# Kernel tuning notes

Measured on AMD Instinct MI355X. Metric: run time of the kernel, lower is better.

The kernel has to match this reference:

```python
import jax, jax.numpy as jnp
import numpy as np

T = 32.0                       # softmax temperature
THRESH = float(np.cos(np.pi * 40.0 / 180.0))  # cos(degree), degree=40
NEG_INF = -9.0e15


def setup_inputs() -> dict:
    key = jax.random.key(0)
    ks = jax.random.split(key, 11)
    B, C, D_IMG, D_ATT, H_ATT, H = 2048, 1000, 2048, 312, 128, 128
    def rn(k, shape, scale=1.0):
        return jax.random.normal(k, shape, dtype=jnp.float32) * scale
    return {
        "image_feats": rn(ks[0], (B, D_IMG)),
        "img_proto":   rn(ks[1], (C, D_IMG)),
        "attributes":  rn(ks[2], (C, D_ATT)),
        "unused":      0,
        # parameters
        "att_g":   rn(ks[3], (D_ATT, H_ATT), 0.05),
        "slim_w":  rn(ks[4], (D_IMG, D_ATT), 0.02),   # proto_slim weight (transposed torch layout)
        "slim_b":  rn(ks[5], (D_ATT,), 0.02),
        "img_w":   rn(ks[6], (D_IMG, H), 0.02),
        "proto_w": rn(ks[7], (2 * D_ATT, H), 0.02),   # att_dim + proto_red_dim = 624
        "proto_b": rn(ks[8], (1, H), 0.02),
        "fc_w":    rn(ks[9], (H, 1), 0.05),
        "fc_b":    rn(ks[10], (1,), 0.05),
    }


def reference(image_feats, img_proto, attributes, unused,
              att_g, slim_w, slim_b, img_w, proto_w, proto_b, fc_w, fc_b):
    # proto_slim: [C, D_img] -> [C, att_dim]
    proto_red = img_proto @ slim_w + slim_b

    # --- get_attention: cosine similarity among attribute projections ---
    g = attributes @ att_g                                   # [C, att_hC] (g == h in original)
    gn = g / jnp.clip(jnp.linalg.norm(g, axis=1, keepdims=True), 1e-12)
    sim = gn @ gn.T                                          # [C, C] cosine similarity
    raw = jnp.where(sim > THRESH, sim, NEG_INF)              # threshold mask
    attn = jax.nn.softmax(raw * T, axis=1)                   # [C, C]

    # --- propagate prototypes ---
    att_outs = attn @ attributes                             # [C, att_dim]
    img_proto_outs = attn @ proto_red                        # [C, att_dim]
    outs = jnp.concatenate([att_outs, img_proto_outs], axis=1)  # [C, 2*att_dim]

    # --- relation MLP (broadcast instead of materialized expand+matmul) ---
    img_h = image_feats @ img_w                              # [B, H]
    proto_h = outs @ proto_w                                 # [C, H]
    hidden = jax.nn.relu(img_h[:, None, :] + proto_h[None, :, :] + proto_b)  # [B, C, H]
    outputs = hidden @ fc_w + fc_b                           # [B, C, 1]
    return outputs[..., 0]                                   # [B, C]
```

## Files before the change

### kernel.cpp

```cpp
#include <hip/hip_runtime.h>

typedef unsigned short ushort_t;
typedef __bf16 bf16x8 __attribute__((ext_vector_type(8)));
typedef float f32x4 __attribute__((ext_vector_type(4)));
typedef float f32x2 __attribute__((ext_vector_type(2)));
typedef ushort_t us4 __attribute__((ext_vector_type(4)));

#define T_SOFT 32.0f
#define THRESH 0.76604444311897803f
#define SW 1048

__device__ __forceinline__ ushort_t f2bf(float f) {
  union { float f; unsigned u; } x; x.f = f;
  unsigned r = (x.u + 0x7fffu + ((x.u >> 16) & 1u)) >> 16;
  return (ushort_t)r;
}
__device__ __forceinline__ float bf2f(ushort_t h) {
  union { unsigned u; float f; } x; x.u = ((unsigned)h) << 16; return x.f;
}

__device__ __forceinline__ us4 pack4(float4 x) {
  union { unsigned u[2]; us4 h; } r;
  union { float4 f; unsigned u[4]; } a;
  a.f = x;
  r.u[0] = __builtin_amdgcn_perm(a.u[1] + 0x8000u, a.u[0] + 0x8000u, 0x07060302u);
  r.u[1] = __builtin_amdgcn_perm(a.u[3] + 0x8000u, a.u[2] + 0x8000u, 0x07060302u);
  return r.h;
}

__global__ __launch_bounds__(256) void tr3_k(const float* __restrict__ s0, ushort_t* __restrict__ d0,
                                             const float* __restrict__ s1, ushort_t* __restrict__ d1,
                                             const float* __restrict__ s2, ushort_t* __restrict__ d2,
                                             const float* __restrict__ s3, ushort_t* __restrict__ d3,
                                             float* __restrict__ z0, float* __restrict__ z1,
                                             ushort_t* __restrict__ gn_bf) {
  int b = blockIdx.x, tid = threadIdx.x;
  if (b >= 1296) {
    if (b < 1360) {
      int local = b - 1296;
      float4 z = make_float4(0.f, 0.f, 0.f, 0.f);
      float4* p = reinterpret_cast<float4*>(z0) + local * 1024 + tid;
      p[0] = z; p[256] = z; p[512] = z; p[768] = z;
    } else if (b < 1437) {
      int local = b - 1360;
      float4 z = make_float4(0.f, 0.f, 0.f, 0.f);
      float4* p = reinterpret_cast<float4*>(z1);
      int base = local * 1024 + tid;
      #pragma unroll
      for (int i = 0; i < 4; ++i) { int idx = base + i * 256; if (idx < 78000) p[idx] = z; }
    } else {
      us4 z = {0, 0, 0, 0};
      *reinterpret_cast<us4*>(gn_bf + 1000 * 128 + tid * 4) = z;
    }
    return;
  }
  __shared__ float tl[32][33];
  const float* src; ushort_t* dst; int R, C, Rpad, local, ctiles;
  if (b < 640)       { src = s0; dst = d0; R = 2048; C = 312; Rpad = 2048; local = b;        ctiles = 10; }
  else if (b < 896)  { src = s1; dst = d1; R = 2048; C = 128; Rpad = 2048; local = b - 640;  ctiles = 4;  }
  else if (b < 976)  { src = s2; dst = d2; R = 624;  C = 128; Rpad = 640;  local = b - 896;  ctiles = 4;  }
  else               { src = s3; dst = d3; R = 1000; C = 312; Rpad = 1024; local = b - 976;  ctiles = 10; }
  int rt = local / ctiles, ct = local - rt * ctiles;
  int r0 = rt * 32, c0 = ct * 32;
  #pragma unroll
  for (int p = 0; p < 4; ++p) {
    int idx = p * 256 + tid;
    int rr = idx >> 5, cc = idx & 31;
    float v = 0.f;
    if (r0 + rr < R && c0 + cc < C) v = src[(size_t)(r0 + rr) * C + (c0 + cc)];
    tl[cc][rr] = v;
  }
  __syncthreads();
  int cc = tid >> 3, rq = tid & 7;
  if (c0 + cc < C) {
    us4 o;
    o[0] = f2bf(tl[cc][rq * 4 + 0]);
    o[1] = f2bf(tl[cc][rq * 4 + 1]);
    o[2] = f2bf(tl[cc][rq * 4 + 2]);
    o[3] = f2bf(tl[cc][rq * 4 + 3]);
    *reinterpret_cast<us4*>(dst + (size_t)(c0 + cc) * Rpad + r0 + rq * 4) = o;
  }
}

template <int NCT>
__device__ __forceinline__ void gemm_seg(
    const float* __restrict__ A, int M, int lda,
    const ushort_t* __restrict__ BT, int ldbt,
    float* __restrict__ C, int N,
    int r0, int c0, int k0, int nsteps,
    ushort_t* __restrict__ As, ushort_t* __restrict__ Bs, int tid) {
  const int SA = 72;
  const int BP = NCT / 2;
  int lane = tid & 63, wv = tid >> 6;
  int l15 = lane & 15, quad = lane >> 4;
  int arow = tid >> 4, akq = tid & 15;
  int brow = tid >> 3, bkq = tid & 7;

  const float* agp[8];
  #pragma unroll
  for (int p = 0; p < 8; ++p) {
    int r = r0 + arow + p * 16; if (r >= M) r = M - 1;
    agp[p] = A + (size_t)r * lda + k0 + akq * 4;
  }
  const ushort_t* bgp[BP];
  #pragma unroll
  for (int p = 0; p < BP; ++p)
    bgp[p] = BT + (size_t)(c0 + brow + p * 32) * ldbt + k0 + bkq * 8;

  float4 ap[8]; bf16x8 bp[BP];
  #pragma unroll
  for (int p = 0; p < 8; ++p) ap[p] = *reinterpret_cast<const float4*>(agp[p]);
  #pragma unroll
  for (int p = 0; p < BP; ++p) bp[p] = *reinterpret_cast<const bf16x8*>(bgp[p]);

  f32x4 acc[2][NCT];
  #pragma unroll
  for (int i = 0; i < 2; ++i)
    #pragma unroll
    for (int j = 0; j < NCT; ++j) acc[i][j] = f32x4{0.f, 0.f, 0.f, 0.f};

  for (int s = 0; s < nsteps; ++s) {
    if (s) __syncthreads();
    #pragma unroll
    for (int p = 0; p < 8; ++p)
      *reinterpret_cast<us4*>(As + (arow + p * 16) * SA + akq * 4) = pack4(ap[p]);
    #pragma unroll
    for (int p = 0; p < BP; ++p)
      *reinterpret_cast<bf16x8*>(Bs + (brow + p * 32) * SA + bkq * 8) = bp[p];
    if (s + 1 < nsteps) {
      #pragma unroll
      for (int p = 0; p < 8; ++p) ap[p] = *reinterpret_cast<const float4*>(agp[p] + 64);
      #pragma unroll
      for (int p = 0; p < BP; ++p) bp[p] = *reinterpret_cast<const bf16x8*>(bgp[p] + 64);
      #pragma unroll
      for (int p = 0; p < 8; ++p) agp[p] += 64;
      #pragma unroll
      for (int p = 0; p < BP; ++p) bgp[p] += 64;
    }
    __syncthreads();
    #pragma unroll
    for (int kh = 0; kh < 2; ++kh) {
      bf16x8 af[2];
      #pragma unroll
      for (int pi = 0; pi < 2; ++pi)
        af[pi] = *reinterpret_cast<bf16x8*>(As + ((wv * 2 + pi) * 16 + l15) * SA + kh * 32 + quad * 8);
      #pragma unroll
      for (int ct = 0; ct < NCT; ++ct) {
        bf16x8 bfr = *reinterpret_cast<bf16x8*>(Bs + (ct * 16 + l15) * SA + kh * 32 + quad * 8);
        acc[0][ct] = __builtin_amdgcn_mfma_f32_16x16x32_bf16(af[0], bfr, acc[0][ct], 0, 0, 0);
        acc[1][ct] = __builtin_amdgcn_mfma_f32_16x16x32_bf16(af[1], bfr, acc[1][ct], 0, 0, 0);
      }
    }
  }
  #pragma unroll
  for (int pi = 0; pi < 2; ++pi) {
    #pragma unroll
    for (int ct = 0; ct < NCT; ++ct) {
      int col = c0 + ct * 16 + l15;
      if (col < N) {
        #pragma unroll
        for (int r = 0; r < 4; ++r) {
          int row = r0 + (wv * 2 + pi) * 16 + quad * 4 + r;
          if (row < M) atomicAdd(&C[(size_t)row * N + col], acc[pi][ct][r]);
        }
      }
    }
  }
}

__global__ __launch_bounds__(256) void mega_k(
    const float* __restrict__ attributes, const float* __restrict__ att_g,
    ushort_t* __restrict__ gn_bf,
    const float* __restrict__ img_proto, const ushort_t* __restrict__ slimT,
    float* __restrict__ proto_red,
    const float* __restrict__ image_feats, const ushort_t* __restrict__ imgwT,
    float* __restrict__ img_h) {
  __shared__ ushort_t As[128 * 72];
  __shared__ ushort_t Bs[128 * 72];
  int b = blockIdx.x, tid = threadIdx.x;
  if (b < 125) {
    __shared__ float a_lds[8][316];
    __shared__ float red2[8][2];
    int h = tid & 127;
    int c0 = b * 8;
    for (int idx = tid; idx < 8 * 312; idx += 256) {
      int r = idx / 312;
      int k = idx - r * 312;
      a_lds[r][k] = attributes[(c0 + r) * 312 + k];
    }
    __syncthreads();
    float acc[8] = {0.f,0.f,0.f,0.f,0.f,0.f,0.f,0.f};
    for (int k = 0; k < 312; k += 4) {
      float w0 = att_g[(k + 0) * 128 + h];
      float w1 = att_g[(k + 1) * 128 + h];
      float w2 = att_g[(k + 2) * 128 + h];
      float w3 = att_g[(k + 3) * 128 + h];
      #pragma unroll
      for (int r = 0; r < 8; ++r) {
        float4 a4 = *reinterpret_cast<const float4*>(&a_lds[r][k]);
        acc[r] += a4.x * w0 + a4.y * w1 + a4.z * w2 + a4.w * w3;
      }
    }
    int lane = tid & 63, wvid = (tid >> 6) & 1;
    #pragma unroll
    for (int r = 0; r < 8; ++r) {
      float v = acc[r] * acc[r];
      #pragma unroll
      for (int off = 32; off > 0; off >>= 1) v += __shfl_xor(v, off, 64);
      if (lane == 0) red2[r][wvid] = v;
    }
    __syncthreads();
    #pragma unroll
    for (int r = 0; r < 8; ++r) {
      float nrm = fmaxf(sqrtf(red2[r][0] + red2[r][1]), 1e-12f);
      gn_bf[(c0 + r) * 128 + h] = f2bf(acc[r] / nrm);
    }
    return;
  }
  b -= 125;
  if (b < 64) {
    int rb = b >> 2, kc = b & 3;
    gemm_seg<8>(image_feats, 2048, 2048, imgwT, 2048, img_h, 128,
                rb * 128, 0, kc * 512, 8, As, Bs, tid);
  } else {
    b -= 64;
    int kc = b & 3; int t = b >> 2;
    int rb = t / 3, cb = t - rb * 3;
    if (cb == 2)
      gemm_seg<4>(img_proto, 1000, 2048, slimT, 2048, proto_red, 312,
                  rb * 128, 256, kc * 512, 8, As, Bs, tid);
    else
      gemm_seg<8>(img_proto, 1000, 2048, slimT, 2048, proto_red, 312,
                  rb * 128, cb * 128, kc * 512, 8, As, Bs, tid);
  }
}

__global__ __launch_bounds__(256) void trp_k(const float* __restrict__ proto_red,
                                             ushort_t* __restrict__ poutT) {
  int b = blockIdx.x, tid = threadIdx.x;
  if (b >= 320) {
    int local = b - 320;
    us4 z = {0, 0, 0, 0};
    ushort_t* base = poutT + 624ull * 1024 + local * 4096;
    *reinterpret_cast<us4*>(base + tid * 16)      = z;
    *reinterpret_cast<us4*>(base + tid * 16 + 4)  = z;
    *reinterpret_cast<us4*>(base + tid * 16 + 8)  = z;
    *reinterpret_cast<us4*>(base + tid * 16 + 12) = z;
    return;
  }
  __shared__ float tl[32][33];
  int rt = b / 10, ct = b - rt * 10;
  int r0 = rt * 32, c0 = ct * 32;
  #pragma unroll
  for (int p = 0; p < 4; ++p) {
    int idx = p * 256 + tid;
    int rr = idx >> 5, cc = idx & 31;
    float v = 0.f;
    if (r0 + rr < 1000 && c0 + cc < 312) v = proto_red[(size_t)(r0 + rr) * 312 + (c0 + cc)];
    tl[cc][rr] = v;
  }
  __syncthreads();
  int cc = tid >> 3, rq = tid & 7;
  if (c0 + cc < 312) {
    us4 o;
    o[0] = f2bf(tl[cc][rq * 4 + 0]);
    o[1] = f2bf(tl[cc][rq * 4 + 1]);
    o[2] = f2bf(tl[cc][rq * 4 + 2]);
    o[3] = f2bf(tl[cc][rq * 4 + 3]);
    *reinterpret_cast<us4*>(poutT + (size_t)(312 + c0 + cc) * 1024 + r0 + rq * 4) = o;
  }
}

__global__ __launch_bounds__(256) void attn3_k(
    const ushort_t* __restrict__ gn_bf, const ushort_t* __restrict__ poutT,
    const float* __restrict__ slim_b, ushort_t* __restrict__ outs) {
  __shared__ ushort_t W[16 * SW];
  __shared__ float rsum[16];
  __shared__ int flags[63];
  int tid = threadIdx.x;
  int i0 = blockIdx.x * 16;
  int lane = tid & 63, wv = tid >> 6;
  int l15 = lane & 15, quad = lane >> 4;
  if (tid < 63) flags[tid] = 0;
  if (tid >= 64 && tid < 80) rsum[tid - 64] = 0.f;
  W[(tid >> 4) * SW + 1008 + (tid & 15)] = 0;
  __syncthreads();

  const ushort_t* abase = gn_bf + (size_t)(i0 + l15) * 128 + quad * 8;
  bf16x8 af0 = *reinterpret_cast<const bf16x8*>(abase);
  bf16x8 af1 = *reinterpret_cast<const bf16x8*>(abase + 32);
  bf16x8 af2 = *reinterpret_cast<const bf16x8*>(abase + 64);
  bf16x8 af3 = *reinterpret_cast<const bf16x8*>(abase + 96);
  float rs[4] = {0.f, 0.f, 0.f, 0.f};
  for (int jt = wv; jt < 63; jt += 4) {
    const ushort_t* bbase = gn_bf + (size_t)(jt * 16 + l15) * 128 + quad * 8;
    f32x4 d = {0.f, 0.f, 0.f, 0.f};
    d = __builtin_amdgcn_mfma_f32_16x16x32_bf16(af0, *reinterpret_cast<const bf16x8*>(bbase),      d, 0, 0, 0);
    d = __builtin_amdgcn_mfma_f32_16x16x32_bf16(af1, *reinterpret_cast<const bf16x8*>(bbase + 32), d, 0, 0, 0);
    d = __builtin_amdgcn_mfma_f32_16x16x32_bf16(af2, *reinterpret_cast<const bf16x8*>(bbase + 64), d, 0, 0, 0);
    d = __builtin_amdgcn_mfma_f32_16x16x32_bf16(af3, *reinterpret_cast<const bf16x8*>(bbase + 96), d, 0, 0, 0);
    int hot = 0;
    #pragma unroll
    for (int r = 0; r < 4; ++r) {
      float w = 0.f;
      if (d[r] > THRESH) { w = __expf(T_SOFT * (d[r] - 1.0f)); hot = 1; }
      ushort_t wb = f2bf(w);
      W[(quad * 4 + r) * SW + jt * 16 + l15] = wb;
      rs[r] += bf2f(wb);
    }
    if (hot) flags[jt] = 1;
  }
  #pragma unroll
  for (int r = 0; r < 4; ++r) {
    float v = rs[r];
    v += __shfl_xor(v, 1, 64); v += __shfl_xor(v, 2, 64);
    v += __shfl_xor(v, 4, 64); v += __shfl_xor(v, 8, 64);
    if (l15 == 0) atomicAdd(&rsum[quad * 4 + r], v);
  }
  __syncthreads();

  f32x4 acc[10];
  #pragma unroll
  for (int t = 0; t < 10; ++t) acc[t] = f32x4{0.f, 0.f, 0.f, 0.f};
  for (int s = 0; s < 32; ++s) {
    int f = flags[2 * s] | ((2 * s + 1 < 63) ? flags[2 * s + 1] : 0);
    if (!f) continue;
    bf16x8 a = *reinterpret_cast<bf16x8*>(W + l15 * SW + s * 32 + quad * 8);
    #pragma unroll
    for (int t = 0; t < 10; ++t) {
      int nrow = (wv * 10 + t) * 16 + l15;
      bf16x8 bfr = *reinterpret_cast<const bf16x8*>(poutT + (size_t)nrow * 1024 + s * 32 + quad * 8);
      acc[t] = __builtin_amdgcn_mfma_f32_16x16x32_bf16(a, bfr, acc[t], 0, 0, 0);
    }
  }
  #pragma unroll
  for (int t = 0; t < 10; ++t) {
    int col = (wv * 10 + t) * 16 + l15;
    float bias = (col >= 312 && col < 624) ? slim_b[col - 312] : 0.f;
    #pragma unroll
    for (int r = 0; r < 4; ++r) {
      int gi = i0 + quad * 4 + r;
      if (gi < 1000) {
        float inv = 1.f / fmaxf(rsum[quad * 4 + r], 1e-30f);
        outs[(size_t)gi * 640 + col] = f2bf(acc[t][r] * inv + bias);
      }
    }
  }
}

__global__ __launch_bounds__(256) void mfma_gemm_bt(
    const ushort_t* __restrict__ A, const ushort_t* __restrict__ BT,
    float* __restrict__ C, int M, int N, int K, int Mt, int Nt,
    const float* __restrict__ bias) {
  int wid = blockIdx.x * 4 + (threadIdx.x >> 6);
  int lane = threadIdx.x & 63;
  int tm = wid / Nt;
  int tn = wid - tm * Nt;
  if (tm >= Mt) return;
  int l15 = lane & 15;
  int quad = lane >> 4;
  const bf16x8* ap = reinterpret_cast<const bf16x8*>(A + (size_t)(tm * 16 + l15) * K + quad * 8);
  const bf16x8* bp = reinterpret_cast<const bf16x8*>(BT + (size_t)(tn * 16 + l15) * K + quad * 8);
  f32x4 acc = {0.f, 0.f, 0.f, 0.f};
  for (int s = 0, steps = K >> 7; s < steps; ++s) {
    bf16x8 a0 = ap[0],  b0 = bp[0];
    bf16x8 a1 = ap[4],  b1 = bp[4];
    bf16x8 a2 = ap[8],  b2 = bp[8];
    bf16x8 a3 = ap[12], b3 = bp[12];
    ap += 16; bp += 16;
    acc = __builtin_amdgcn_mfma_f32_16x16x32_bf16(a0, b0, acc, 0, 0, 0);
    acc = __builtin_amdgcn_mfma_f32_16x16x32_bf16(a1, b1, acc, 0, 0, 0);
    acc = __builtin_amdgcn_mfma_f32_16x16x32_bf16(a2, b2, acc, 0, 0, 0);
    acc = __builtin_amdgcn_mfma_f32_16x16x32_bf16(a3, b3, acc, 0, 0, 0);
  }
  int col = tn * 16 + l15;
  if (col >= N) return;
  float bv = bias ? bias[col] : 0.f;
  int row0 = tm * 16 + quad * 4;
  #pragma unroll
  for (int r = 0; r < 4; ++r) {
    int row = row0 + r;
    if (row < M) C[(size_t)row * N + col] = acc[r] + bv;
  }
}

__global__ __launch_bounds__(256) void final_k(
    const float* __restrict__ img_h, const float* __restrict__ ph,
    const float* __restrict__ fc_w, const float* __restrict__ fc_b,
    float* __restrict__ out) {
  __shared__ float ih[128][132];
  __shared__ float ps[64][132];
  __shared__ float ws_[128];
  int tid = threadIdx.x;
  int b0 = blockIdx.x * 128;
  int c0 = blockIdx.y * 64;
  for (int idx = tid; idx < 4096; idx += 256) {
    int row = idx >> 5, c4 = (idx & 31) * 4;
    float4 v = *reinterpret_cast<const float4*>(img_h + (size_t)(b0 + row) * 128 + c4);
    *reinterpret_cast<float4*>(&ih[row][c4]) = v;
  }
  for (int idx = tid; idx < 2048; idx += 256) {
    int row = idx >> 5, c4 = (idx & 31) * 4;
    int c = c0 + row;
    float4 v = make_float4(0.f, 0.f, 0.f, 0.f);
    if (c < 1000) v = *reinterpret_cast<const float4*>(ph + (size_t)c * 128 + c4);
    *reinterpret_cast<float4*>(&ps[row][c4]) = v;
  }
  if (tid < 128) ws_[tid] = fc_w[tid];
  __syncthreads();
  int tx = tid & 15, ty = tid >> 4;
  f32x2 acc[8][4] = {};
  const f32x2 zero2 = {0.f, 0.f};
  for (int h = 0; h < 128; h += 4) {
    float4 w4 = *reinterpret_cast<float4*>(&ws_[h]);
    f32x2 wlo = {w4.x, w4.y}, whi = {w4.z, w4.w};
    float4 a4[8], p4[4];
    #pragma unroll
    for (int i = 0; i < 8; ++i) a4[i] = *reinterpret_cast<float4*>(&ih[ty * 8 + i][h]);
    #pragma unroll
    for (int j = 0; j < 4; ++j) p4[j] = *reinterpret_cast<float4*>(&ps[tx * 4 + j][h]);
    #pragma unroll
    for (int i = 0; i < 8; ++i) {
      f32x2 alo = {a4[i].x, a4[i].y}, ahi = {a4[i].z, a4[i].w};
      #pragma unroll
      for (int j = 0; j < 4; ++j) {
        f32x2 plo = {p4[j].x, p4[j].y}, phi = {p4[j].z, p4[j].w};
        f32x2 t0 = __builtin_elementwise_max(alo + plo, zero2);
        f32x2 t1 = __builtin_elementwise_max(ahi + phi, zero2);
        acc[i][j] = acc[i][j] + t0 * wlo;
        acc[i][j] = acc[i][j] + t1 * whi;
      }
    }
  }
  float fb = fc_b[0];
  #pragma unroll
  for (int i = 0; i < 8; ++i) {
    int b = b0 + ty * 8 + i;
    int c = c0 + tx * 4;
    if (c < 1000) {
      float4 v = make_float4(acc[i][0].x + acc[i][0].y + fb, acc[i][1].x + acc[i][1].y + fb,
                             acc[i][2].x + acc[i][2].y + fb, acc[i][3].x + acc[i][3].y + fb);
      *reinterpret_cast<float4*>(out + (size_t)b * 1000 + c) = v;
    }
  }
}

extern "C" void kernel_launch(void* const* d_in, const int* in_sizes, int n_in,
                              void* d_out, int out_size, void* d_ws, size_t ws_size,
                              hipStream_t stream) {
  const float* image_feats = (const float*)d_in[0];
  const float* img_proto   = (const float*)d_in[1];
  const float* attributes  = (const float*)d_in[2];
  const float* att_g   = (const float*)d_in[4];
  const float* slim_w  = (const float*)d_in[5];
  const float* slim_b  = (const float*)d_in[6];
  const float* img_w   = (const float*)d_in[7];
  const float* proto_w = (const float*)d_in[8];
  const float* proto_b = (const float*)d_in[9];
  const float* fc_w    = (const float*)d_in[10];
  const float* fc_b    = (const float*)d_in[11];
  float* out = (float*)d_out;

  char* ws = (char*)d_ws;
  size_t o = 0;
  auto alloc = [&](size_t bytes) { size_t r = o; o += (bytes + 255) & ~(size_t)255; return r; };
  ushort_t* imgwT   = (ushort_t*)(ws + alloc(128ull * 2048 * 2));
  ushort_t* slimT   = (ushort_t*)(ws + alloc(320ull * 2048 * 2));
  ushort_t* protowT = (ushort_t*)(ws + alloc(128ull * 640 * 2));
  ushort_t* gn_bf   = (ushort_t*)(ws + alloc(1008ull * 128 * 2));
  float* proto_red = (float*)(ws + alloc(1000ull * 312 * 4));
  ushort_t* poutT   = (ushort_t*)(ws + alloc(640ull * 1024 * 2));
  ushort_t* outs_bf = (ushort_t*)(ws + alloc(1008ull * 640 * 2));
  float* img_h     = (float*)(ws + alloc(2048ull * 128 * 4));
  float* ph        = (float*)(ws + alloc(1000ull * 128 * 4));

  tr3_k<<<1438, 256, 0, stream>>>(slim_w, slimT, img_w, imgwT, proto_w, protowT,
                                  attributes, poutT, img_h, proto_red, gn_bf);

  mega_k<<<285, 256, 0, stream>>>(attributes, att_g, gn_bf,
                                  img_proto, slimT, proto_red,
                                  image_feats, imgwT, img_h);

  trp_k<<<324, 256, 0, stream>>>(proto_red, poutT);

  attn3_k<<<63, 256, 0, stream>>>(gn_bf, poutT, slim_b, outs_bf);

  mfma_gemm_bt<<<126, 256, 0, stream>>>(outs_bf, protowT, ph, 1000, 128, 640, 63, 8, proto_b);

  final_k<<<dim3(16, 16), 256, 0, stream>>>(img_h, ph, fc_w, fc_b, out);
}
```

Before: 182.7 us.

## Fuse proto transpose into GEMM, drop split-K atomics, fuse proto_w GEMM into attention

The proto_red GEMM is now computed in transposed form (slimT times img_proto^T) and written straight to poutT as bf16, which removes the separate transpose kernel and the fp32 proto_red buffer. The img_h and proto GEMMs no longer split K four ways with atomicAdd, so the zeroing blocks go away, but each block now runs the full K=2048 loop with fewer blocks in flight. The outs @ proto_w GEMM is fused into the attention kernel through a shared-memory staging tile, which removes the outs_bf round trip and one launch. Together this cuts the pipeline from six launches to four, at the cost of less parallelism in the big GEMMs.

```diff
diff --git a/kernel.cpp b/kernel.cpp
--- a/kernel.cpp
+++ b/kernel.cpp
@@ -9,6 +9,7 @@
 #define T_SOFT 32.0f
 #define THRESH 0.76604444311897803f
 #define SW 1048
+#define SO 648
 
 __device__ __forceinline__ ushort_t f2bf(float f) {
   union { float f; unsigned u; } x; x.f = f;
@@ -32,34 +33,25 @@
                                              const float* __restrict__ s1, ushort_t* __restrict__ d1,
                                              const float* __restrict__ s2, ushort_t* __restrict__ d2,
                                              const float* __restrict__ s3, ushort_t* __restrict__ d3,
-                                             float* __restrict__ z0, float* __restrict__ z1,
-                                             ushort_t* __restrict__ gn_bf) {
+                                             ushort_t* __restrict__ gn_bf, ushort_t* __restrict__ poutT) {
   int b = blockIdx.x, tid = threadIdx.x;
   if (b >= 1296) {
-    if (b < 1360) {
-      int local = b - 1296;
-      float4 z = make_float4(0.f, 0.f, 0.f, 0.f);
-      float4* p = reinterpret_cast<float4*>(z0) + local * 1024 + tid;
-      p[0] = z; p[256] = z; p[512] = z; p[768] = z;
-    } else if (b < 1437) {
-      int local = b - 1360;
-      float4 z = make_float4(0.f, 0.f, 0.f, 0.f);
-      float4* p = reinterpret_cast<float4*>(z1);
-      int base = local * 1024 + tid;
-      #pragma unroll
-      for (int i = 0; i < 4; ++i) { int idx = base + i * 256; if (idx < 78000) p[idx] = z; }
+    us4 z = {0, 0, 0, 0};
+    if (b == 1296) {
+      *reinterpret_cast<us4*>(gn_bf + 1000 * 128 + tid * 4) = z;
     } else {
-      us4 z = {0, 0, 0, 0};
-      *reinterpret_cast<us4*>(gn_bf + 1000 * 128 + tid * 4) = z;
+      ushort_t* base = poutT + 632ull * 1024 + tid * 32;
+      #pragma unroll
+      for (int i = 0; i < 8; ++i) *reinterpret_cast<us4*>(base + i * 4) = z;
     }
     return;
   }
   __shared__ float tl[32][33];
-  const float* src; ushort_t* dst; int R, C, Rpad, local, ctiles;
-  if (b < 640)       { src = s0; dst = d0; R = 2048; C = 312; Rpad = 2048; local = b;        ctiles = 10; }
-  else if (b < 896)  { src = s1; dst = d1; R = 2048; C = 128; Rpad = 2048; local = b - 640;  ctiles = 4;  }
-  else if (b < 976)  { src = s2; dst = d2; R = 624;  C = 128; Rpad = 640;  local = b - 896;  ctiles = 4;  }
-  else               { src = s3; dst = d3; R = 1000; C = 312; Rpad = 1024; local = b - 976;  ctiles = 10; }
+  const float* src; ushort_t* dst; int R, C, Cw, Rpad, local, ctiles;
+  if (b < 640)       { src = s0; dst = d0; R = 2048; C = 312; Cw = 320; Rpad = 2048; local = b;       ctiles = 10; }
+  else if (b < 896)  { src = s1; dst = d1; R = 2048; C = 128; Cw = 128; Rpad = 2048; local = b - 640; ctiles = 4;  }
+  else if (b < 976)  { src = s2; dst = d2; R = 624;  C = 128; Cw = 128; Rpad = 640;  local = b - 896; ctiles = 4;  }
+  else               { src = s3; dst = d3; R = 1000; C = 312; Cw = 312; Rpad = 1024; local = b - 976; ctiles = 10; }
   int rt = local / ctiles, ct = local - rt * ctiles;
   int r0 = rt * 32, c0 = ct * 32;
   #pragma unroll
@@ -72,7 +64,7 @@
   }
   __syncthreads();
   int cc = tid >> 3, rq = tid & 7;
-  if (c0 + cc < C) {
+  if (c0 + cc < Cw) {
     us4 o;
     o[0] = f2bf(tl[cc][rq * 4 + 0]);
     o[1] = f2bf(tl[cc][rq * 4 + 1]);
@@ -82,60 +74,50 @@
   }
 }
 
-template <int NCT>
-__device__ __forceinline__ void gemm_seg(
-    const float* __restrict__ A, int M, int lda,
-    const ushort_t* __restrict__ BT, int ldbt,
-    float* __restrict__ C, int N,
-    int r0, int c0, int k0, int nsteps,
-    ushort_t* __restrict__ As, ushort_t* __restrict__ Bs, int tid) {
+__device__ __forceinline__ void gemm_imgh(const float* __restrict__ A, const ushort_t* __restrict__ BT,
+                                          float* __restrict__ C, int r0,
+                                          ushort_t* __restrict__ As, ushort_t* __restrict__ Bs, int tid) {
   const int SA = 72;
-  const int BP = NCT / 2;
   int lane = tid & 63, wv = tid >> 6;
   int l15 = lane & 15, quad = lane >> 4;
   int arow = tid >> 4, akq = tid & 15;
   int brow = tid >> 3, bkq = tid & 7;
-
   const float* agp[8];
   #pragma unroll
-  for (int p = 0; p < 8; ++p) {
-    int r = r0 + arow + p * 16; if (r >= M) r = M - 1;
-    agp[p] = A + (size_t)r * lda + k0 + akq * 4;
-  }
-  const ushort_t* bgp[BP];
-  #pragma unroll
-  for (int p = 0; p < BP; ++p)
-    bgp[p] = BT + (size_t)(c0 + brow + p * 32) * ldbt + k0 + bkq * 8;
-
-  float4 ap[8]; bf16x8 bp[BP];
+  for (int p = 0; p < 8; ++p) agp[p] = A + (size_t)(r0 + arow + p * 16) * 2048 + akq * 4;
+  const ushort_t* bgp[4];
+  #pragma unroll
+  for (int p = 0; p < 4; ++p) bgp[p] = BT + (size_t)(brow + p * 32) * 2048 + bkq * 8;
+
+  float4 ap[8]; bf16x8 bp[4];
   #pragma unroll
   for (int p = 0; p < 8; ++p) ap[p] = *reinterpret_cast<const float4*>(agp[p]);
   #pragma unroll
-  for (int p = 0; p < BP; ++p) bp[p] = *reinterpret_cast<const bf16x8*>(bgp[p]);
-
-  f32x4 acc[2][NCT];
+  for (int p = 0; p < 4; ++p) bp[p] = *reinterpret_cast<const bf16x8*>(bgp[p]);
+
+  f32x4 acc[2][8];
   #pragma unroll
   for (int i = 0; i < 2; ++i)
     #pragma unroll
-    for (int j = 0; j < NCT; ++j) acc[i][j] = f32x4{0.f, 0.f, 0.f, 0.f};
-
-  for (int s = 0; s < nsteps; ++s) {
+    for (int j = 0; j < 8; ++j) acc[i][j] = f32x4{0.f, 0.f, 0.f, 0.f};
+
+  for (int s = 0; s < 32; ++s) {
     if (s) __syncthreads();
     #pragma unroll
     for (int p = 0; p < 8; ++p)
       *reinterpret_cast<us4*>(As + (arow + p * 16) * SA + akq * 4) = pack4(ap[p]);
     #pragma unroll
-    for (int p = 0; p < BP; ++p)
+    for (int p = 0; p < 4; ++p)
       *reinterpret_cast<bf16x8*>(Bs + (brow + p * 32) * SA + bkq * 8) = bp[p];
-    if (s + 1 < nsteps) {
+    if (s + 1 < 32) {
       #pragma unroll
       for (int p = 0; p < 8; ++p) ap[p] = *reinterpret_cast<const float4*>(agp[p] + 64);
       #pragma unroll
-      for (int p = 0; p < BP; ++p) bp[p] = *reinterpret_cast<const bf16x8*>(bgp[p] + 64);
+      for (int p = 0; p < 4; ++p) bp[p] = *reinterpret_cast<const bf16x8*>(bgp[p] + 64);
       #pragma unroll
       for (int p = 0; p < 8; ++p) agp[p] += 64;
       #pragma unroll
-      for (int p = 0; p < BP; ++p) bgp[p] += 64;
+      for (int p = 0; p < 4; ++p) bgp[p] += 64;
     }
     __syncthreads();
     #pragma unroll
@@ -145,7 +127,7 @@
       for (int pi = 0; pi < 2; ++pi)
         af[pi] = *reinterpret_cast<bf16x8*>(As + ((wv * 2 + pi) * 16 + l15) * SA + kh * 32 + quad * 8);
       #pragma unroll
-      for (int ct = 0; ct < NCT; ++ct) {
+      for (int ct = 0; ct < 8; ++ct) {
         bf16x8 bfr = *reinterpret_cast<bf16x8*>(Bs + (ct * 16 + l15) * SA + kh * 32 + quad * 8);
         acc[0][ct] = __builtin_amdgcn_mfma_f32_16x16x32_bf16(af[0], bfr, acc[0][ct], 0, 0, 0);
         acc[1][ct] = __builtin_amdgcn_mfma_f32_16x16x32_bf16(af[1], bfr, acc[1][ct], 0, 0, 0);
@@ -153,28 +135,104 @@
     }
   }
   #pragma unroll
-  for (int pi = 0; pi < 2; ++pi) {
-    #pragma unroll
-    for (int ct = 0; ct < NCT; ++ct) {
-      int col = c0 + ct * 16 + l15;
-      if (col < N) {
+  for (int pi = 0; pi < 2; ++pi)
+    #pragma unroll
+    for (int ct = 0; ct < 8; ++ct) {
+      int col = ct * 16 + l15;
+      #pragma unroll
+      for (int r = 0; r < 4; ++r) {
+        int row = r0 + (wv * 2 + pi) * 16 + quad * 4 + r;
+        C[(size_t)row * 128 + col] = acc[pi][ct][r];
+      }
+    }
+}
+
+__device__ __forceinline__ void gemm_protoT(const ushort_t* __restrict__ A, const float* __restrict__ B,
+                                            ushort_t* __restrict__ poutT, int r0, int c0,
+                                            ushort_t* __restrict__ As, ushort_t* __restrict__ Bs, int tid) {
+  const int SA = 72;
+  int lane = tid & 63, wv = tid >> 6;
+  int l15 = lane & 15, quad = lane >> 4;
+  int frow = tid >> 4, fkq = tid & 15;
+  int hrow = tid >> 3, hkq = tid & 7;
+  const ushort_t* agp[4];
+  #pragma unroll
+  for (int p = 0; p < 4; ++p) {
+    int r = r0 + hrow + p * 32; if (r >= 320) r = 319;
+    agp[p] = A + (size_t)r * 2048 + hkq * 8;
+  }
+  const float* bgp[8];
+  #pragma unroll
+  for (int p = 0; p < 8; ++p) {
+    int n = c0 + frow + p * 16; if (n >= 1000) n = 999;
+    bgp[p] = B + (size_t)n * 2048 + fkq * 4;
+  }
+  bf16x8 ar[4]; float4 br[8];
+  #pragma unroll
+  for (int p = 0; p < 4; ++p) ar[p] = *reinterpret_cast<const bf16x8*>(agp[p]);
+  #pragma unroll
+  for (int p = 0; p < 8; ++p) br[p] = *reinterpret_cast<const float4*>(bgp[p]);
+
+  f32x4 acc[2][8];
+  #pragma unroll
+  for (int i = 0; i < 2; ++i)
+    #pragma unroll
+    for (int j = 0; j < 8; ++j) acc[i][j] = f32x4{0.f, 0.f, 0.f, 0.f};
+
+  for (int s = 0; s < 32; ++s) {
+    if (s) __syncthreads();
+    #pragma unroll
+    for (int p = 0; p < 4; ++p)
+      *reinterpret_cast<bf16x8*>(As + (hrow + p * 32) * SA + hkq * 8) = ar[p];
+    #pragma unroll
+    for (int p = 0; p < 8; ++p)
+      *reinterpret_cast<us4*>(Bs + (frow + p * 16) * SA + fkq * 4) = pack4(br[p]);
+    if (s + 1 < 32) {
+      #pragma unroll
+      for (int p = 0; p < 4; ++p) ar[p] = *reinterpret_cast<const bf16x8*>(agp[p] + 64);
+      #pragma unroll
+      for (int p = 0; p < 8; ++p) br[p] = *reinterpret_cast<const float4*>(bgp[p] + 64);
+      #pragma unroll
+      for (int p = 0; p < 4; ++p) agp[p] += 64;
+      #pragma unroll
+      for (int p = 0; p < 8; ++p) bgp[p] += 64;
+    }
+    __syncthreads();
+    #pragma unroll
+    for (int kh = 0; kh < 2; ++kh) {
+      bf16x8 af[2];
+      #pragma unroll
+      for (int pi = 0; pi < 2; ++pi)
+        af[pi] = *reinterpret_cast<bf16x8*>(As + ((wv * 2 + pi) * 16 + l15) * SA + kh * 32 + quad * 8);
+      #pragma unroll
+      for (int ct = 0; ct < 8; ++ct) {
+        bf16x8 bfr = *reinterpret_cast<bf16x8*>(Bs + (ct * 16 + l15) * SA + kh * 32 + quad * 8);
+        acc[0][ct] = __builtin_amdgcn_mfma_f32_16x16x32_bf16(af[0], bfr, acc[0][ct], 0, 0, 0);
+        acc[1][ct] = __builtin_amdgcn_mfma_f32_16x16x32_bf16(af[1], bfr, acc[1][ct], 0, 0, 0);
+      }
+    }
+  }
+  #pragma unroll
+  for (int pi = 0; pi < 2; ++pi)
+    #pragma unroll
+    for (int ct = 0; ct < 8; ++ct) {
+      int n = c0 + ct * 16 + l15;
+      if (n < 1000) {
         #pragma unroll
         for (int r = 0; r < 4; ++r) {
-          int row = r0 + (wv * 2 + pi) * 16 + quad * 4 + r;
-          if (row < M) atomicAdd(&C[(size_t)row * N + col], acc[pi][ct][r]);
+          int m = r0 + (wv * 2 + pi) * 16 + quad * 4 + r;
+          if (m < 320) poutT[(size_t)(312 + m) * 1024 + n] = f2bf(acc[pi][ct][r]);
         }
       }
     }
-  }
 }
 
 __global__ __launch_bounds__(256) void mega_k(
     const float* __restrict__ attributes, const float* __restrict__ att_g,
     ushort_t* __restrict__ gn_bf,
     const float* __restrict__ img_proto, const ushort_t* __restrict__ slimT,
-    float* __restrict__ proto_red,
     const float* __restrict__ image_feats, const ushort_t* __restrict__ imgwT,
-    float* __restrict__ img_h) {
+    float* __restrict__ img_h, ushort_t* __restrict__ poutT) {
   __shared__ ushort_t As[128 * 72];
   __shared__ ushort_t Bs[128 * 72];
   int b = blockIdx.x, tid = threadIdx.x;
@@ -218,63 +276,21 @@
     return;
   }
   b -= 125;
-  if (b < 64) {
-    int rb = b >> 2, kc = b & 3;
-    gemm_seg<8>(image_feats, 2048, 2048, imgwT, 2048, img_h, 128,
-                rb * 128, 0, kc * 512, 8, As, Bs, tid);
+  if (b < 16) {
+    gemm_imgh(image_feats, imgwT, img_h, b * 128, As, Bs, tid);
   } else {
-    b -= 64;
-    int kc = b & 3; int t = b >> 2;
-    int rb = t / 3, cb = t - rb * 3;
-    if (cb == 2)
-      gemm_seg<4>(img_proto, 1000, 2048, slimT, 2048, proto_red, 312,
-                  rb * 128, 256, kc * 512, 8, As, Bs, tid);
-    else
-      gemm_seg<8>(img_proto, 1000, 2048, slimT, 2048, proto_red, 312,
-                  rb * 128, cb * 128, kc * 512, 8, As, Bs, tid);
-  }
-}
-
-__global__ __launch_bounds__(256) void trp_k(const float* __restrict__ proto_red,
-                                             ushort_t* __restrict__ poutT) {
-  int b = blockIdx.x, tid = threadIdx.x;
-  if (b >= 320) {
-    int local = b - 320;
-    us4 z = {0, 0, 0, 0};
-    ushort_t* base = poutT + 624ull * 1024 + local * 4096;
-    *reinterpret_cast<us4*>(base + tid * 16)      = z;
-    *reinterpret_cast<us4*>(base + tid * 16 + 4)  = z;
-    *reinterpret_cast<us4*>(base + tid * 16 + 8)  = z;
-    *reinterpret_cast<us4*>(base + tid * 16 + 12) = z;
-    return;
-  }
-  __shared__ float tl[32][33];
-  int rt = b / 10, ct = b - rt * 10;
-  int r0 = rt * 32, c0 = ct * 32;
-  #pragma unroll
-  for (int p = 0; p < 4; ++p) {
-    int idx = p * 256 + tid;
-    int rr = idx >> 5, cc = idx & 31;
-    float v = 0.f;
-    if (r0 + rr < 1000 && c0 + cc < 312) v = proto_red[(size_t)(r0 + rr) * 312 + (c0 + cc)];
-    tl[cc][rr] = v;
-  }
-  __syncthreads();
-  int cc = tid >> 3, rq = tid & 7;
-  if (c0 + cc < 312) {
-    us4 o;
-    o[0] = f2bf(tl[cc][rq * 4 + 0]);
-    o[1] = f2bf(tl[cc][rq * 4 + 1]);
-    o[2] = f2bf(tl[cc][rq * 4 + 2]);
-    o[3] = f2bf(tl[cc][rq * 4 + 3]);
-    *reinterpret_cast<us4*>(poutT + (size_t)(312 + c0 + cc) * 1024 + r0 + rq * 4) = o;
-  }
-}
-
-__global__ __launch_bounds__(256) void attn3_k(
+    b -= 16;
+    int rb = b >> 3, cb = b & 7;
+    gemm_protoT(slimT, img_proto, poutT, rb * 128, cb * 128, As, Bs, tid);
+  }
+}
+
+__global__ __launch_bounds__(256) void attn4_k(
     const ushort_t* __restrict__ gn_bf, const ushort_t* __restrict__ poutT,
-    const float* __restrict__ slim_b, ushort_t* __restrict__ outs) {
+    const float* __restrict__ slim_b, const ushort_t* __restrict__ protowT,
+    const float* __restrict__ proto_b, float* __restrict__ ph) {
   __shared__ ushort_t W[16 * SW];
+  __shared__ ushort_t OS[16 * SO];
   __shared__ float rsum[16];
   __shared__ int flags[63];
   int tid = threadIdx.x;
@@ -339,48 +355,34 @@
     float bias = (col >= 312 && col < 624) ? slim_b[col - 312] : 0.f;
     #pragma unroll
     for (int r = 0; r < 4; ++r) {
+      int row = quad * 4 + r;
+      float inv = 1.f / fmaxf(rsum[row], 1e-30f);
+      OS[row * SO + col] = f2bf(acc[t][r] * inv + bias);
+    }
+  }
+  __syncthreads();
+
+  f32x4 acc2[2];
+  acc2[0] = f32x4{0.f, 0.f, 0.f, 0.f};
+  acc2[1] = f32x4{0.f, 0.f, 0.f, 0.f};
+  for (int s = 0; s < 20; ++s) {
+    bf16x8 a = *reinterpret_cast<bf16x8*>(OS + l15 * SO + s * 32 + quad * 8);
+    #pragma unroll
+    for (int t = 0; t < 2; ++t) {
+      int n = (wv * 2 + t) * 16 + l15;
+      bf16x8 bfr = *reinterpret_cast<const bf16x8*>(protowT + (size_t)n * 640 + s * 32 + quad * 8);
+      acc2[t] = __builtin_amdgcn_mfma_f32_16x16x32_bf16(a, bfr, acc2[t], 0, 0, 0);
+    }
+  }
+  #pragma unroll
+  for (int t = 0; t < 2; ++t) {
+    int h = (wv * 2 + t) * 16 + l15;
+    float pb = proto_b[h];
+    #pragma unroll
+    for (int r = 0; r < 4; ++r) {
       int gi = i0 + quad * 4 + r;
-      if (gi < 1000) {
-        float inv = 1.f / fmaxf(rsum[quad * 4 + r], 1e-30f);
-        outs[(size_t)gi * 640 + col] = f2bf(acc[t][r] * inv + bias);
-      }
-    }
-  }
-}
-
-__global__ __launch_bounds__(256) void mfma_gemm_bt(
-    const ushort_t* __restrict__ A, const ushort_t* __restrict__ BT,
-    float* __restrict__ C, int M, int N, int K, int Mt, int Nt,
-    const float* __restrict__ bias) {
-  int wid = blockIdx.x * 4 + (threadIdx.x >> 6);
-  int lane = threadIdx.x & 63;
-  int tm = wid / Nt;
-  int tn = wid - tm * Nt;
-  if (tm >= Mt) return;
-  int l15 = lane & 15;
-  int quad = lane >> 4;
-  const bf16x8* ap = reinterpret_cast<const bf16x8*>(A + (size_t)(tm * 16 + l15) * K + quad * 8);
-  const bf16x8* bp = reinterpret_cast<const bf16x8*>(BT + (size_t)(tn * 16 + l15) * K + quad * 8);
-  f32x4 acc = {0.f, 0.f, 0.f, 0.f};
-  for (int s = 0, steps = K >> 7; s < steps; ++s) {
-    bf16x8 a0 = ap[0],  b0 = bp[0];
-    bf16x8 a1 = ap[4],  b1 = bp[4];
-    bf16x8 a2 = ap[8],  b2 = bp[8];
-    bf16x8 a3 = ap[12], b3 = bp[12];
-    ap += 16; bp += 16;
-    acc = __builtin_amdgcn_mfma_f32_16x16x32_bf16(a0, b0, acc, 0, 0, 0);
-    acc = __builtin_amdgcn_mfma_f32_16x16x32_bf16(a1, b1, acc, 0, 0, 0);
-    acc = __builtin_amdgcn_mfma_f32_16x16x32_bf16(a2, b2, acc, 0, 0, 0);
-    acc = __builtin_amdgcn_mfma_f32_16x16x32_bf16(a3, b3, acc, 0, 0, 0);
-  }
-  int col = tn * 16 + l15;
-  if (col >= N) return;
-  float bv = bias ? bias[col] : 0.f;
-  int row0 = tm * 16 + quad * 4;
-  #pragma unroll
-  for (int r = 0; r < 4; ++r) {
-    int row = row0 + r;
-    if (row < M) C[(size_t)row * N + col] = acc[r] + bv;
+      if (gi < 1000) ph[(size_t)gi * 128 + h] = acc2[t][r] + pb;
+    }
   }
 }
 
@@ -468,24 +470,18 @@
   ushort_t* slimT   = (ushort_t*)(ws + alloc(320ull * 2048 * 2));
   ushort_t* protowT = (ushort_t*)(ws + alloc(128ull * 640 * 2));
   ushort_t* gn_bf   = (ushort_t*)(ws + alloc(1008ull * 128 * 2));
-  float* proto_red = (float*)(ws + alloc(1000ull * 312 * 4));
   ushort_t* poutT   = (ushort_t*)(ws + alloc(640ull * 1024 * 2));
-  ushort_t* outs_bf = (ushort_t*)(ws + alloc(1008ull * 640 * 2));
   float* img_h     = (float*)(ws + alloc(2048ull * 128 * 4));
   float* ph        = (float*)(ws + alloc(1000ull * 128 * 4));
 
-  tr3_k<<<1438, 256, 0, stream>>>(slim_w, slimT, img_w, imgwT, proto_w, protowT,
-                                  attributes, poutT, img_h, proto_red, gn_bf);
-
-  mega_k<<<285, 256, 0, stream>>>(attributes, att_g, gn_bf,
-                                  img_proto, slimT, proto_red,
-                                  image_feats, imgwT, img_h);
-
-  trp_k<<<324, 256, 0, stream>>>(proto_red, poutT);
-
-  attn3_k<<<63, 256, 0, stream>>>(gn_bf, poutT, slim_b, outs_bf);
-
-  mfma_gemm_bt<<<126, 256, 0, stream>>>(outs_bf, protowT, ph, 1000, 128, 640, 63, 8, proto_b);
+  tr3_k<<<1298, 256, 0, stream>>>(slim_w, slimT, img_w, imgwT, proto_w, protowT,
+                                  attributes, poutT, gn_bf, poutT);
+
+  mega_k<<<165, 256, 0, stream>>>(attributes, att_g, gn_bf,
+                                  img_proto, slimT,
+                                  image_feats, imgwT, img_h, poutT);
+
+  attn4_k<<<63, 256, 0, stream>>>(gn_bf, poutT, slim_b, protowT, proto_b, ph);
 
   final_k<<<dim3(16, 16), 256, 0, stream>>>(img_h, ph, fc_w, fc_b, out);
 }
```

New measurement: 175.7 us. 3.8% less time.
